# Performance work log

Measured on AMD Instinct MI355X. Metric: run time of the kernel, lower is better.

Reference implementation:

```python
import jax, jax.numpy as jnp
import numpy as np

H, W = 32, 32
C = 512
HEADS = 8
HEAD_DIM = C // HEADS
B = 8
GROUPS = 32
EPS = 1e-6
N = H * W


def _rel_indices():
    # (N, N) lookup indices into the (2H-1)*(2W-1) relative-position table
    y = np.arange(H)
    x = np.arange(W)
    y1, x1, y2, x2 = np.meshgrid(y, x, y, x, indexing='ij')
    idx = (y1 - y2 + H - 1) * (2 * W - 1) + (x1 - x2 + W - 1)
    return jnp.asarray(idx.reshape(N, N), dtype=jnp.int32)

REL_IDX = _rel_indices()


def setup_inputs() -> dict:
    key = jax.random.key(0)
    ks = jax.random.split(key, 8)
    s = 0.02
    return {
        'x': jax.random.normal(ks[0], (B, C, H, W), jnp.float32),
        '_1': jnp.zeros((1,), jnp.int32),
        '_2': jnp.zeros((1,), jnp.int32),
        'gamma': jnp.ones((C,), jnp.float32),
        'beta': jnp.zeros((C,), jnp.float32),
        'wq': jax.random.normal(ks[1], (C, C), jnp.float32) * s,
        'bq': jnp.zeros((C,), jnp.float32),
        'wk': jax.random.normal(ks[2], (C, C), jnp.float32) * s,
        'bk': jnp.zeros((C,), jnp.float32),
        'wv': jax.random.normal(ks[3], (C, C), jnp.float32) * s,
        'bv': jnp.zeros((C,), jnp.float32),
        'wproj': jax.random.normal(ks[4], (C, C), jnp.float32) * s,
        'bproj': jnp.zeros((C,), jnp.float32),
        'pos_enc': jax.random.normal(ks[5], (HEADS, (2 * H - 1) * (2 * W - 1)), jnp.float32) * s,
    }


def _group_norm(x, gamma, beta):
    b, c, h, w = x.shape
    xg = x.reshape(b, GROUPS, c // GROUPS, h, w)
    mean = xg.mean(axis=(2, 3, 4), keepdims=True)
    var = xg.var(axis=(2, 3, 4), keepdims=True)
    xg = (xg - mean) * jax.lax.rsqrt(var + EPS)
    x = xg.reshape(b, c, h, w)
    return x * gamma[None, :, None, None] + beta[None, :, None, None]


def reference(x, _1, _2, gamma, beta, wq, bq, wk, bk, wv, bv, wproj, bproj, pos_enc):
    x0 = x
    xn = _group_norm(x, gamma, beta)
    xt = xn.reshape(B, C, N)  # (B, C, N)

    def proj(w, bias):
        # 1x1 conv == channel matmul: (B, C_out, N)
        y = jnp.einsum('oc,bcn->bon', w, xt) + bias[None, :, None]
        # split heads: channel index = head*HEAD_DIM + d -> (B, heads, N, d)
        return y.reshape(B, HEADS, HEAD_DIM, N).transpose(0, 1, 3, 2)

    q = proj(wq, bq)
    k = proj(wk, bk)
    v = proj(wv, bv)

    scale = 1.0 / jnp.sqrt(jnp.float32(HEAD_DIM))
    attn = jnp.einsum('bhqd,bhkd->bhqk', q, k) * scale  # (B, heads, N, N)
    rel_bias = pos_enc[:, REL_IDX]  # (heads, N, N)
    attn = attn + rel_bias[None]
    attn = jax.nn.softmax(attn, axis=-1)

    out = jnp.einsum('bhqk,bhkd->bhqd', attn, v)  # (B, heads, N, d)
    out = out.transpose(0, 1, 3, 2).reshape(B, C, H, W)
    out = jnp.einsum('oc,bchw->bohw', wproj, out) + bproj[None, :, None, None]
    return out + x0
```

## Files before the change

kernel.cpp:

```cpp
#include <hip/hip_runtime.h>
#include <hip/hip_bf16.h>
#include <math.h>

typedef __bf16 bf16_t;
typedef __bf16 bf16x8 __attribute__((ext_vector_type(8)));
typedef __bf16 bf16x4 __attribute__((ext_vector_type(4)));
typedef float  f32x4  __attribute__((ext_vector_type(4)));

#define MFMA16(a, b, c) __builtin_amdgcn_mfma_f32_16x16x32_bf16((a), (b), (c), 0, 0, 0)
#define GLDS16(g, s) __builtin_amdgcn_global_load_lds( \
    (const __attribute__((address_space(1))) void*)(g), \
    (__attribute__((address_space(3))) void*)(s), 16, 0, 0)

#define LOG2E 1.4426950408889634f

__global__ __launch_bounds__(512) void prep_kernel(
    const float* __restrict__ wq, const float* __restrict__ wk,
    const float* __restrict__ wv, const float* __restrict__ wp,
    bf16_t* __restrict__ Wqkv, bf16_t* __restrict__ Wp,
    const float* __restrict__ pos, bf16_t* __restrict__ Bias2,
    const float* __restrict__ x, const float* __restrict__ gamma,
    const float* __restrict__ beta, bf16_t* __restrict__ xnT)
{
    const int blk = blockIdx.x;
    const int t = threadIdx.x;
    __shared__ __align__(16) char pshm[4096];

    if (blk < 512) {
        bf16_t* ps = (bf16_t*)pshm;
        const int h   = blk >> 6;
        const int qt  = blk & 63;
        const int qy  = qt >> 1;
        const int qxb = (qt & 1) * 16;
        for (int i = t; i < 32 * 63; i += 512) {
            const int r = i / 63, dx = i - r * 63;
            ps[r * 64 + dx] = (bf16_t)(pos[h * 3969 + (qy + r) * 63 + dx] * LOG2E);
        }
        __syncthreads();
        bf16_t* outb = Bias2 + (((size_t)h * 64 + qt) * 64) * 256;
#pragma unroll
        for (int it = 0; it < 8; ++it) {
            const int idx = t + it * 512;
            const int kt = idx >> 6, l = idx & 63;
            const int qx  = qxb + (l & 15);
            const int nk0 = kt * 16 + (l >> 4) * 4;
            const int ky = nk0 >> 5;
            const int kx0 = nk0 & 31;
            const int r = 31 - ky;
            const int dx0 = qx - kx0 + 31;
            bf16x4 o;
#pragma unroll
            for (int j = 0; j < 4; ++j) o[j] = ps[r * 64 + dx0 - j];
            *(bf16x4*)(outb + (size_t)idx * 4) = o;
        }
    } else if (blk < 768) {
        float* red = (float*)pshm;
        const int bgn = blk - 512;
        const int b = bgn >> 5, g = bgn & 31;
        const int hi = t >> 8, tl = t & 255;
        const float* base = x + ((size_t)b * 512 + g * 16) * 1024;

        f32x4 v[8];
        float s = 0.f, s2 = 0.f;
#pragma unroll
        for (int it = 0; it < 8; ++it) {
            v[it] = *(const f32x4*)(base + (size_t)hi * 8192 + it * 1024 + tl * 4);
#pragma unroll
            for (int j = 0; j < 4; ++j) { s += v[it][j]; s2 += v[it][j] * v[it][j]; }
        }
#pragma unroll
        for (int m = 1; m < 64; m <<= 1) { s += __shfl_xor(s, m); s2 += __shfl_xor(s2, m); }
        const int w = t >> 6;
        if ((t & 63) == 0) { red[w] = s; red[8 + w] = s2; }
        __syncthreads();
        s = 0.f; s2 = 0.f;
#pragma unroll
        for (int i = 0; i < 8; ++i) { s += red[i]; s2 += red[8 + i]; }
        const float mean = s * (1.f / 16384.f);
        const float var  = fmaxf(s2 * (1.f / 16384.f) - mean * mean, 0.f);
        const float rstd = rsqrtf(var + 1e-6f);

        float ga[8], be[8];
#pragma unroll
        for (int it = 0; it < 8; ++it) {
            const int gc = g * 16 + hi * 8 + it;
            ga[it] = gamma[gc] * rstd;
            be[it] = beta[gc] - mean * ga[it];
        }
#pragma unroll
        for (int j = 0; j < 4; ++j) {
            bf16x8 o;
#pragma unroll
            for (int it = 0; it < 8; ++it)
                o[it] = (bf16_t)(v[it][j] * ga[it] + be[it]);
            *(bf16x8*)(xnT + ((size_t)b * 1024 + tl * 4 + j) * 512 + g * 16 + hi * 8) = o;
        }
    } else {
        const int i = ((blk - 768) * 512 + t) * 4;
#pragma unroll
        for (int j = 0; j < 4; ++j) {
            Wqkv[i + j]          = (bf16_t)wq[i + j];
            Wqkv[262144 + i + j] = (bf16_t)wk[i + j];
            Wqkv[524288 + i + j] = (bf16_t)wv[i + j];
            Wp[i + j]            = (bf16_t)wp[i + j];
        }
    }
}

__global__ __launch_bounds__(256) void gemm_bt(
    const bf16_t* __restrict__ A, const bf16_t* __restrict__ Bt, int mode,
    int mtiles,
    const float* __restrict__ bias0, const float* __restrict__ bias1,
    const float* __restrict__ bias2,
    const float* __restrict__ x0, float* __restrict__ outF,
    bf16_t* __restrict__ Qb, bf16_t* __restrict__ Kb, bf16_t* __restrict__ Vb)
{
    const int K  = 512;
    const int g  = blockIdx.x;
    const int xcd = g & 7;
    const int i_  = g >> 3;
    const int m_idx = i_ % mtiles;
    const int n_idx = xcd * 8 + i_ / mtiles;
    const int m0 = m_idx * 128;
    const int n0 = n_idx * 128;
    const int t = threadIdx.x;
    const int l = t & 63, w = t >> 6;
    const int wr = w >> 1, wc = w & 1;
    const int lrow = l & 15, lgrp = l >> 4;

    __shared__ __align__(16) char smem_raw[49152];
    bf16_t* Ct = (bf16_t*)smem_raw;

    f32x4 acc[4][4];
#pragma unroll
    for (int i = 0; i < 4; ++i)
#pragma unroll
        for (int j = 0; j < 4; ++j) acc[i][j] = (f32x4){0.f, 0.f, 0.f, 0.f};

    const bf16_t* gA0 = A  + (size_t)(m0 + w * 16 + (l >> 2)) * K + (l & 3) * 8;
    const bf16_t* gA1 = gA0 + (size_t)64 * K;
    const bf16_t* gB0 = Bt + (size_t)(n0 + w * 16 + (l >> 2)) * K + (l & 3) * 8;
    const bf16_t* gB1 = gB0 + (size_t)64 * K;

#define STAGE(s, k0) do {                                                   \
    bf16_t* As_ = (bf16_t*)(smem_raw + (s) * 16384);                        \
    bf16_t* Bs_ = (bf16_t*)(smem_raw + (s) * 16384 + 8192);                 \
    GLDS16(gA0 + (k0), As_ + w * 512);                                      \
    GLDS16(gA1 + (k0), As_ + 2048 + w * 512);                               \
    GLDS16(gB0 + (k0), Bs_ + w * 512);                                      \
    GLDS16(gB1 + (k0), Bs_ + 2048 + w * 512); } while (0)

    STAGE(0, 0);
    STAGE(1, 32);

#pragma unroll
    for (int tk = 0; tk < 16; ++tk) {
        if (tk < 15) asm volatile("s_waitcnt vmcnt(4)" ::: "memory");
        else         asm volatile("s_waitcnt vmcnt(0)" ::: "memory");
        __builtin_amdgcn_s_barrier();
        __builtin_amdgcn_sched_barrier(0);
        if (tk + 2 < 16) STAGE((tk + 2) % 3, (tk + 2) * 32);
        const bf16_t* Asb = (const bf16_t*)(smem_raw + (tk % 3) * 16384);
        const bf16_t* Bsb = Asb + 4096;
        bf16x8 af[4], bfr[4];
#pragma unroll
        for (int ms = 0; ms < 4; ++ms)
            af[ms] = *(const bf16x8*)&Asb[(wr * 64 + ms * 16 + lrow) * 32 + lgrp * 8];
#pragma unroll
        for (int ns = 0; ns < 4; ++ns)
            bfr[ns] = *(const bf16x8*)&Bsb[(wc * 64 + ns * 16 + lrow) * 32 + lgrp * 8];
        __builtin_amdgcn_s_setprio(1);
#pragma unroll
        for (int ms = 0; ms < 4; ++ms)
#pragma unroll
            for (int ns = 0; ns < 4; ++ns)
                acc[ms][ns] = MFMA16(af[ms], bfr[ns], acc[ms][ns]);
        __builtin_amdgcn_s_setprio(0);
    }
#undef STAGE

    if (mode == 0) {
        const int which = m0 >> 9;
        const int mq = (m0 >> 7) & 3;
        const float* bias = (which == 0) ? bias0 : (which == 1) ? bias1 : bias2;
        const float scl = (which == 0) ? 0.125f * LOG2E : 1.0f;
        const int b   = n_idx >> 3;
        const int nn0 = (n_idx & 7) * 128;

        __syncthreads();
        if (which < 2) {
            bf16_t* Qk = (which == 0) ? Qb : Kb;
#pragma unroll
            for (int ms = 0; ms < 4; ++ms) {
                const int ml = wr * 64 + ms * 16 + lgrp * 4;
#pragma unroll
                for (int ns = 0; ns < 4; ++ns) {
                    const int nl = wc * 64 + ns * 16 + lrow;
                    bf16x4 pk;
#pragma unroll
                    for (int j = 0; j < 4; ++j)
                        pk[j] = (bf16_t)((acc[ms][ns][j] + bias[mq * 128 + ml + j]) * scl);
                    *(bf16x4*)&Ct[nl * 136 + ml] = pk;
                }
            }
            __syncthreads();
#pragma unroll
            for (int it = 0; it < 8; ++it) {
                const int idx = it * 256 + t;
                const int token = idx >> 4, oc = idx & 15;
                const bf16x8 vv8 = *(const bf16x8*)&Ct[token * 136 + oc * 8];
                const int head = mq * 2 + (oc >> 3);
                const int d = (oc & 7) * 8;
                *(bf16x8*)(Qk + (((size_t)b * 8 + head) * 1024 + nn0 + token) * 64 + d) = vv8;
            }
        } else {
#pragma unroll
            for (int ms = 0; ms < 4; ++ms) {
                const int ml = wr * 64 + ms * 16 + lgrp * 4;
#pragma unroll
                for (int ns = 0; ns < 4; ++ns) {
                    const int nl = wc * 64 + ns * 16 + lrow;
#pragma unroll
                    for (int j = 0; j < 4; ++j)
                        Ct[(ml + j) * 136 + nl] =
                            (bf16_t)(acc[ms][ns][j] + bias[mq * 128 + ml + j]);
                }
            }
            __syncthreads();
#pragma unroll
            for (int it = 0; it < 8; ++it) {
                const int idx = it * 256 + t;
                const int o = idx >> 4, nc = idx & 15;
                const bf16x8 vv8 = *(const bf16x8*)&Ct[o * 136 + nc * 8];
                const int head = mq * 2 + (o >> 6);
                const int d = o & 63;
                *(bf16x8*)(Vb + (((size_t)b * 8 + head) * 64 + d) * 1024 + nn0 + nc * 8) = vv8;
            }
        }
    } else {
#pragma unroll
        for (int ms = 0; ms < 4; ++ms) {
#pragma unroll
            for (int ns = 0; ns < 4; ++ns) {
                const int c  = m0 + wr * 64 + ms * 16 + lgrp * 4;
                const int np = n0 + wc * 64 + ns * 16 + lrow;
                const int b = np >> 10, n = np & 1023;
#pragma unroll
                for (int j = 0; j < 4; ++j) {
                    const size_t idx = ((size_t)b * 512 + c + j) * 1024 + n;
                    outF[idx] = acc[ms][ns][j] + bias0[c + j] + x0[idx];
                }
            }
        }
    }
}

__global__ __launch_bounds__(512) void attn_kernel(
    const bf16_t* __restrict__ Qb, const bf16_t* __restrict__ Kb,
    const bf16_t* __restrict__ Vb, const bf16_t* __restrict__ Bias2,
    bf16_t* __restrict__ Xo)
{
    const int bh = blockIdx.x;
    const int h  = bh & 7;
    const int q0 = blockIdx.y * 128;
    const int t = threadIdx.x;
    const int w = t >> 6, l = t & 63;
    const int lrow = l & 15, lgrp = l >> 4;

    __shared__ __align__(16) bf16_t Ks[128][72];
    __shared__ __align__(16) bf16_t Vs[64][136];
    __shared__ __align__(16) bf16_t Ps[8][16][72];

    const int qrow = q0 + w * 16 + lrow;
    const bf16_t* qbase = Qb + ((size_t)bh * 1024 + qrow) * 64;
    const bf16x8 qf0 = *(const bf16x8*)(qbase + lgrp * 8);
    const bf16x8 qf1 = *(const bf16x8*)(qbase + 32 + lgrp * 8);

    const bf16_t* bb = Bias2 + (((size_t)h * 64 + (q0 >> 4) + w) * 64) * 256;

    bf16x8 ones;
#pragma unroll
    for (int i = 0; i < 8; ++i) ones[i] = (bf16_t)1.0f;

    f32x4 oacc[4], tsacc = (f32x4){0.f, 0.f, 0.f, 0.f};
#pragma unroll
    for (int j = 0; j < 4; ++j) oacc[j] = (f32x4){0.f, 0.f, 0.f, 0.f};

    const int sr2 = t >> 3;
    const int sc2 = (t & 7) * 8;
    const bf16_t* Kg = Kb + ((size_t)bh * 1024 + sr2) * 64 + sc2;
    const bf16_t* Vg = Vb + ((size_t)bh * 64 + sr2) * 1024 + sc2;

    bf16x8 kv0 = *(const bf16x8*)(Kg);
    bf16x8 kv1 = *(const bf16x8*)(Kg + (size_t)64 * 64);
    bf16x8 vv0 = *(const bf16x8*)(Vg);
    bf16x8 vv1 = *(const bf16x8*)(Vg + 64);
    bf16x4 bA[8], bB[8];
#pragma unroll
    for (int k = 0; k < 8; ++k)
        bA[k] = *(const bf16x4*)(bb + (size_t)(k * 64 + l) * 4);

    auto dtile = [&](int it, bf16x4 (&bcur)[8], bf16x4 (&bnxt)[8]) {
        const int nk0 = it * 128;
        __syncthreads();
        *(bf16x8*)&Ks[sr2][sc2]      = kv0;
        *(bf16x8*)&Ks[64 + sr2][sc2] = kv1;
        *(bf16x8*)&Vs[sr2][sc2]      = vv0;
        *(bf16x8*)&Vs[sr2][64 + sc2] = vv1;
        __syncthreads();
        if (it < 7) {
            const int nkn = nk0 + 128;
#pragma unroll
            for (int k = 0; k < 8; ++k)
                bnxt[k] = *(const bf16x4*)(bb + (size_t)((((nkn >> 4)) + k) * 64 + l) * 4);
            kv0 = *(const bf16x8*)(Kg + (size_t)nkn * 64);
            kv1 = *(const bf16x8*)(Kg + (size_t)(nkn + 64) * 64);
            vv0 = *(const bf16x8*)(Vg + nkn);
            vv1 = *(const bf16x8*)(Vg + nkn + 64);
        }

#pragma unroll
        for (int st = 0; st < 2; ++st) {
            f32x4 s[4];
#pragma unroll
            for (int ns = 0; ns < 4; ++ns) {
                const bf16x4 bc = bcur[st * 4 + ns];
                f32x4 z = (f32x4){(float)bc[0], (float)bc[1],
                                  (float)bc[2], (float)bc[3]};
                const bf16x8 kf0 = *(const bf16x8*)&Ks[st * 64 + ns * 16 + lrow][lgrp * 8];
                const bf16x8 kf1 = *(const bf16x8*)&Ks[st * 64 + ns * 16 + lrow][32 + lgrp * 8];
                z = MFMA16(kf0, qf0, z);
                z = MFMA16(kf1, qf1, z);
                s[ns] = z;
            }
#pragma unroll
            for (int ns = 0; ns < 4; ++ns) {
                bf16x4 pk;
                pk[0] = (bf16_t)exp2f(s[ns][0]);
                pk[1] = (bf16_t)exp2f(s[ns][1]);
                pk[2] = (bf16_t)exp2f(s[ns][2]);
                pk[3] = (bf16_t)exp2f(s[ns][3]);
                *(bf16x4*)&Ps[w][lrow][ns * 16 + lgrp * 4] = pk;
            }
            const bf16x8 pf0 = *(const bf16x8*)&Ps[w][lrow][lgrp * 8];
            const bf16x8 pf1 = *(const bf16x8*)&Ps[w][lrow][32 + lgrp * 8];
            tsacc = MFMA16(ones, pf0, tsacc);
            tsacc = MFMA16(ones, pf1, tsacc);
#pragma unroll
            for (int ds = 0; ds < 4; ++ds) {
                const bf16x8 vf0 = *(const bf16x8*)&Vs[ds * 16 + lrow][st * 64 + lgrp * 8];
                const bf16x8 vf1 = *(const bf16x8*)&Vs[ds * 16 + lrow][st * 64 + 32 + lgrp * 8];
                oacc[ds] = MFMA16(vf0, pf0, oacc[ds]);
                oacc[ds] = MFMA16(vf1, pf1, oacc[ds]);
            }
        }
    };

    for (int it2 = 0; it2 < 8; it2 += 2) {
        dtile(it2,     bA, bB);
        dtile(it2 + 1, bB, bA);
    }

    const float inv = 1.0f / tsacc[0];

    const int b = bh >> 3;
    const int q = q0 + w * 16 + lrow;
    bf16_t* xrow = Xo + ((size_t)b * 1024 + q) * 512 + h * 64;
#pragma unroll
    for (int ds = 0; ds < 4; ++ds) {
        bf16x4 o4;
#pragma unroll
        for (int j = 0; j < 4; ++j) o4[j] = (bf16_t)(oacc[ds][j] * inv);
        *(bf16x4*)(xrow + ds * 16 + lgrp * 4) = o4;
    }
}

extern "C" void kernel_launch(void* const* d_in, const int* in_sizes, int n_in,
                              void* d_out, int out_size, void* d_ws, size_t ws_size,
                              hipStream_t stream)
{
    const float* x     = (const float*)d_in[0];
    const float* gamma = (const float*)d_in[3];
    const float* beta  = (const float*)d_in[4];
    const float* wq    = (const float*)d_in[5];
    const float* bq    = (const float*)d_in[6];
    const float* wk    = (const float*)d_in[7];
    const float* bk    = (const float*)d_in[8];
    const float* wv    = (const float*)d_in[9];
    const float* bv    = (const float*)d_in[10];
    const float* wp    = (const float*)d_in[11];
    const float* bp    = (const float*)d_in[12];
    const float* pos   = (const float*)d_in[13];
    float* out = (float*)d_out;

    size_t off = 0;
    char* wsb = (char*)d_ws;
    auto alloc = [&](size_t bytes) { char* p = wsb + off; off += bytes; return p; };
    bf16_t* Wqkv  = (bf16_t*)alloc((size_t)1536 * 512 * 2);
    bf16_t* Wp    = (bf16_t*)alloc((size_t)512 * 512 * 2);
    bf16_t* xnT   = (bf16_t*)alloc((size_t)8192 * 512 * 2);
    bf16_t* Qb    = (bf16_t*)alloc((size_t)8192 * 512 * 2);
    bf16_t* Kb    = (bf16_t*)alloc((size_t)8192 * 512 * 2);
    bf16_t* Vb    = (bf16_t*)alloc((size_t)8192 * 512 * 2);
    bf16_t* Xo    = (bf16_t*)alloc((size_t)8192 * 512 * 2);
    bf16_t* Bias2 = (bf16_t*)alloc((size_t)8 * 64 * 64 * 64 * 4 * 2);

    hipLaunchKernelGGL(prep_kernel, dim3(896), dim3(512), 0, stream,
                       wq, wk, wv, wp, Wqkv, Wp, pos, Bias2,
                       x, gamma, beta, xnT);
    hipLaunchKernelGGL(gemm_bt, dim3(768), dim3(256), 0, stream,
                       Wqkv, xnT, 0, 12, bq, bk, bv,
                       nullptr, nullptr, Qb, Kb, Vb);
    hipLaunchKernelGGL(attn_kernel, dim3(64, 8), dim3(512), 0, stream,
                       Qb, Kb, Vb, Bias2, Xo);
    hipLaunchKernelGGL(gemm_bt, dim3(256), dim3(256), 0, stream,
                       Wp, Xo, 1, 4, bp, nullptr, nullptr,
                       x, out, nullptr, nullptr, nullptr);
}
```

Before: 86.11 us.

## Split attention key range across wave halves to double grid size

Each attention block now covers 64 queries instead of 128. The two halves of the 8 waves each take half of every 128-key tile, and their partial outputs and row sums are combined through shared memory at the end. The grid doubles from 512 to 1024 blocks to improve occupancy and CU utilisation. In exchange, every block still loads full K/V tiles for half as many queries, which doubles K/V global traffic and adds an extra sync and reduction step.

Result: slower. 91.88 us (+6.7%).

```diff
diff --git a/kernel.cpp b/kernel.cpp
--- a/kernel.cpp
+++ b/kernel.cpp
@@ -262,21 +262,24 @@
 {
     const int bh = blockIdx.x;
     const int h  = bh & 7;
-    const int q0 = blockIdx.y * 128;
+    const int q0 = blockIdx.y * 64;
     const int t = threadIdx.x;
     const int w = t >> 6, l = t & 63;
+    const int qc = w & 3, half = w >> 2;
     const int lrow = l & 15, lgrp = l >> 4;
 
-    __shared__ __align__(16) bf16_t Ks[128][72];
-    __shared__ __align__(16) bf16_t Vs[64][136];
-    __shared__ __align__(16) bf16_t Ps[8][16][72];
-
-    const int qrow = q0 + w * 16 + lrow;
+    __shared__ __align__(16) char smem[54272];
+    bf16_t* Ks = (bf16_t*)smem;
+    bf16_t* Vs = (bf16_t*)(smem + 18432);
+    bf16_t* Ps = (bf16_t*)(smem + 35840);
+    float*  comb = (float*)smem;
+
+    const int qrow = q0 + qc * 16 + lrow;
     const bf16_t* qbase = Qb + ((size_t)bh * 1024 + qrow) * 64;
     const bf16x8 qf0 = *(const bf16x8*)(qbase + lgrp * 8);
     const bf16x8 qf1 = *(const bf16x8*)(qbase + 32 + lgrp * 8);
 
-    const bf16_t* bb = Bias2 + (((size_t)h * 64 + (q0 >> 4) + w) * 64) * 256;
+    const bf16_t* bb = Bias2 + (((size_t)h * 64 + (q0 >> 4) + qc) * 64) * 256;
 
     bf16x8 ones;
 #pragma unroll
@@ -295,64 +298,60 @@
     bf16x8 kv1 = *(const bf16x8*)(Kg + (size_t)64 * 64);
     bf16x8 vv0 = *(const bf16x8*)(Vg);
     bf16x8 vv1 = *(const bf16x8*)(Vg + 64);
-    bf16x4 bA[8], bB[8];
-#pragma unroll
-    for (int k = 0; k < 8; ++k)
-        bA[k] = *(const bf16x4*)(bb + (size_t)(k * 64 + l) * 4);
-
-    auto dtile = [&](int it, bf16x4 (&bcur)[8], bf16x4 (&bnxt)[8]) {
-        const int nk0 = it * 128;
+    bf16x4 bA[4], bB[4];
+#pragma unroll
+    for (int k = 0; k < 4; ++k)
+        bA[k] = *(const bf16x4*)(bb + (size_t)((half * 4 + k) * 64 + l) * 4);
+
+    auto dtile = [&](int it, bf16x4 (&bcur)[4], bf16x4 (&bnxt)[4]) {
         __syncthreads();
-        *(bf16x8*)&Ks[sr2][sc2]      = kv0;
-        *(bf16x8*)&Ks[64 + sr2][sc2] = kv1;
-        *(bf16x8*)&Vs[sr2][sc2]      = vv0;
-        *(bf16x8*)&Vs[sr2][64 + sc2] = vv1;
+        *(bf16x8*)&Ks[sr2 * 72 + sc2]        = kv0;
+        *(bf16x8*)&Ks[(64 + sr2) * 72 + sc2] = kv1;
+        *(bf16x8*)&Vs[sr2 * 136 + sc2]       = vv0;
+        *(bf16x8*)&Vs[sr2 * 136 + 64 + sc2]  = vv1;
         __syncthreads();
         if (it < 7) {
-            const int nkn = nk0 + 128;
-#pragma unroll
-            for (int k = 0; k < 8; ++k)
-                bnxt[k] = *(const bf16x4*)(bb + (size_t)((((nkn >> 4)) + k) * 64 + l) * 4);
+            const int nkn = (it + 1) * 128;
+#pragma unroll
+            for (int k = 0; k < 4; ++k)
+                bnxt[k] = *(const bf16x4*)(bb + (size_t)(((it + 1) * 8 + half * 4 + k) * 64 + l) * 4);
             kv0 = *(const bf16x8*)(Kg + (size_t)nkn * 64);
             kv1 = *(const bf16x8*)(Kg + (size_t)(nkn + 64) * 64);
             vv0 = *(const bf16x8*)(Vg + nkn);
             vv1 = *(const bf16x8*)(Vg + nkn + 64);
         }
 
-#pragma unroll
-        for (int st = 0; st < 2; ++st) {
-            f32x4 s[4];
-#pragma unroll
-            for (int ns = 0; ns < 4; ++ns) {
-                const bf16x4 bc = bcur[st * 4 + ns];
-                f32x4 z = (f32x4){(float)bc[0], (float)bc[1],
-                                  (float)bc[2], (float)bc[3]};
-                const bf16x8 kf0 = *(const bf16x8*)&Ks[st * 64 + ns * 16 + lrow][lgrp * 8];
-                const bf16x8 kf1 = *(const bf16x8*)&Ks[st * 64 + ns * 16 + lrow][32 + lgrp * 8];
-                z = MFMA16(kf0, qf0, z);
-                z = MFMA16(kf1, qf1, z);
-                s[ns] = z;
-            }
-#pragma unroll
-            for (int ns = 0; ns < 4; ++ns) {
-                bf16x4 pk;
-                pk[0] = (bf16_t)exp2f(s[ns][0]);
-                pk[1] = (bf16_t)exp2f(s[ns][1]);
-                pk[2] = (bf16_t)exp2f(s[ns][2]);
-                pk[3] = (bf16_t)exp2f(s[ns][3]);
-                *(bf16x4*)&Ps[w][lrow][ns * 16 + lgrp * 4] = pk;
-            }
-            const bf16x8 pf0 = *(const bf16x8*)&Ps[w][lrow][lgrp * 8];
-            const bf16x8 pf1 = *(const bf16x8*)&Ps[w][lrow][32 + lgrp * 8];
-            tsacc = MFMA16(ones, pf0, tsacc);
-            tsacc = MFMA16(ones, pf1, tsacc);
-#pragma unroll
-            for (int ds = 0; ds < 4; ++ds) {
-                const bf16x8 vf0 = *(const bf16x8*)&Vs[ds * 16 + lrow][st * 64 + lgrp * 8];
-                const bf16x8 vf1 = *(const bf16x8*)&Vs[ds * 16 + lrow][st * 64 + 32 + lgrp * 8];
-                oacc[ds] = MFMA16(vf0, pf0, oacc[ds]);
-                oacc[ds] = MFMA16(vf1, pf1, oacc[ds]);
-            }
+        f32x4 s[4];
+#pragma unroll
+        for (int ns = 0; ns < 4; ++ns) {
+            const bf16x4 bc = bcur[ns];
+            f32x4 z = (f32x4){(float)bc[0], (float)bc[1],
+                              (float)bc[2], (float)bc[3]};
+            const bf16x8 kf0 = *(const bf16x8*)&Ks[(half * 64 + ns * 16 + lrow) * 72 + lgrp * 8];
+            const bf16x8 kf1 = *(const bf16x8*)&Ks[(half * 64 + ns * 16 + lrow) * 72 + 32 + lgrp * 8];
+            z = MFMA16(kf0, qf0, z);
+            z = MFMA16(kf1, qf1, z);
+            s[ns] = z;
+        }
+#pragma unroll
+        for (int ns = 0; ns < 4; ++ns) {
+            bf16x4 pk;
+            pk[0] = (bf16_t)exp2f(s[ns][0]);
+            pk[1] = (bf16_t)exp2f(s[ns][1]);
+            pk[2] = (bf16_t)exp2f(s[ns][2]);
+            pk[3] = (bf16_t)exp2f(s[ns][3]);
+            *(bf16x4*)&Ps[(w * 16 + lrow) * 72 + ns * 16 + lgrp * 4] = pk;
+        }
+        const bf16x8 pf0 = *(const bf16x8*)&Ps[(w * 16 + lrow) * 72 + lgrp * 8];
+        const bf16x8 pf1 = *(const bf16x8*)&Ps[(w * 16 + lrow) * 72 + 32 + lgrp * 8];
+        tsacc = MFMA16(ones, pf0, tsacc);
+        tsacc = MFMA16(ones, pf1, tsacc);
+#pragma unroll
+        for (int ds = 0; ds < 4; ++ds) {
+            const bf16x8 vf0 = *(const bf16x8*)&Vs[(ds * 16 + lrow) * 136 + half * 64 + lgrp * 8];
+            const bf16x8 vf1 = *(const bf16x8*)&Vs[(ds * 16 + lrow) * 136 + half * 64 + 32 + lgrp * 8];
+            oacc[ds] = MFMA16(vf0, pf0, oacc[ds]);
+            oacc[ds] = MFMA16(vf1, pf1, oacc[ds]);
         }
     };
 
@@ -361,17 +360,35 @@
         dtile(it2 + 1, bB, bA);
     }
 
-    const float inv = 1.0f / tsacc[0];
-
-    const int b = bh >> 3;
-    const int q = q0 + w * 16 + lrow;
-    bf16_t* xrow = Xo + ((size_t)b * 1024 + q) * 512 + h * 64;
-#pragma unroll
-    for (int ds = 0; ds < 4; ++ds) {
-        bf16x4 o4;
-#pragma unroll
-        for (int j = 0; j < 4; ++j) o4[j] = (bf16_t)(oacc[ds][j] * inv);
-        *(bf16x4*)(xrow + ds * 16 + lgrp * 4) = o4;
+    __syncthreads();
+    if (half == 1) {
+        float* p = comb + ((size_t)qc * 64 + l) * 20;
+#pragma unroll
+        for (int ds = 0; ds < 4; ++ds)
+            *(f32x4*)(p + ds * 4) = oacc[ds];
+        p[16] = tsacc[0];
+    }
+    __syncthreads();
+    if (half == 0) {
+        const float* p = comb + ((size_t)qc * 64 + l) * 20;
+#pragma unroll
+        for (int ds = 0; ds < 4; ++ds) {
+            const f32x4 o2 = *(const f32x4*)(p + ds * 4);
+#pragma unroll
+            for (int j = 0; j < 4; ++j) oacc[ds][j] += o2[j];
+        }
+        const float inv = 1.0f / (tsacc[0] + p[16]);
+
+        const int b = bh >> 3;
+        const int q = q0 + qc * 16 + lrow;
+        bf16_t* xrow = Xo + ((size_t)b * 1024 + q) * 512 + h * 64;
+#pragma unroll
+        for (int ds = 0; ds < 4; ++ds) {
+            bf16x4 o4;
+#pragma unroll
+            for (int j = 0; j < 4; ++j) o4[j] = (bf16_t)(oacc[ds][j] * inv);
+            *(bf16x4*)(xrow + ds * 16 + lgrp * 4) = o4;
+        }
     }
 }
 
@@ -411,7 +428,7 @@
     hipLaunchKernelGGL(gemm_bt, dim3(768), dim3(256), 0, stream,
                        Wqkv, xnT, 0, 12, bq, bk, bv,
                        nullptr, nullptr, Qb, Kb, Vb);
-    hipLaunchKernelGGL(attn_kernel, dim3(64, 8), dim3(512), 0, stream,
+    hipLaunchKernelGGL(attn_kernel, dim3(64, 16), dim3(512), 0, stream,
                        Qb, Kb, Vb, Bias2, Xo);
     hipLaunchKernelGGL(gemm_bt, dim3(256), dim3(256), 0, stream,
                        Wp, Xo, 1, 4, bp, nullptr, nullptr,
```
